# Optimization experiments

Measured on AMD Instinct MI355X. Metric: run time of the kernel, lower is better.

Reference implementation:

```python
import jax, jax.numpy as jnp
import numpy as np

BQ, BK = 128, 64  # SpargeAttn-style Q/K block sizes
NEG = -1e30


def _block_mask(q, k, simthreshd1, cdfthreshd, scale):
    """Mean-similarity block selection: a (q-block, k-block) pair is pruned only
    when both blocks are self-similar (mean cosine sim to block mean exceeds the
    per-head simthreshd1) AND it is not in the top-CDF mass (cdfthreshd) of the
    compressed block-level softmax."""
    B, H, L, D = q.shape
    nq, nk = L // BQ, L // BK
    qb = q.reshape(B, H, nq, BQ, D)
    kb = k.reshape(B, H, nk, BK, D)
    qm = qb.mean(3)  # [B,H,nq,D] block means
    km = kb.mean(3)  # [B,H,nk,D]

    def blocksim(xb, xm):
        xn = xb / (jnp.linalg.norm(xb, axis=-1, keepdims=True) + 1e-6)
        mn = xm / (jnp.linalg.norm(xm, axis=-1, keepdims=True) + 1e-6)
        return jnp.einsum('bhntd,bhnd->bhnt', xn, mn).mean(-1)  # [B,H,n]

    th = simthreshd1[None, :, None]
    comp_q = blocksim(qb, qm) > th  # [B,H,nq] self-similar q blocks
    comp_k = blocksim(kb, km) > th  # [B,H,nk]

    # compressed attention over block means, then CDF-based top-mass selection
    p = jax.nn.softmax(jnp.einsum('bhqd,bhkd->bhqk', qm, km) * scale, axis=-1)
    order = jnp.argsort(-p, axis=-1)
    sp = jnp.take_along_axis(p, order, axis=-1)
    csum = jnp.cumsum(sp, axis=-1)
    keep_sorted = (csum - sp) < cdfthreshd[None, :, None, None]  # prefix covering tau
    rank = jnp.argsort(order, axis=-1)  # inverse permutation
    selected = jnp.take_along_axis(keep_sorted, rank, axis=-1)  # [B,H,nq,nk]

    return selected | ~(comp_q[..., :, None] & comp_k[..., None, :])


def setup_inputs() -> dict:
    key = jax.random.key(0)
    kq, kk, kv, kc = jax.random.split(key, 4)
    B, H, L, D = 1, 16, 2048, 64
    return {
        'q': jax.random.normal(kq, (B, H, L, D), dtype=jnp.float32),
        'k': jax.random.normal(kk, (B, H, L, D), dtype=jnp.float32),
        'v': jax.random.normal(kv, (B, H, L, D), dtype=jnp.float32),
        'simthreshd1': jnp.zeros((H,), dtype=jnp.float32),
        'cdfthreshd': jax.random.uniform(kc, (H,), dtype=jnp.float32),
    }


def reference(q, k, v, simthreshd1, cdfthreshd):
    B, H, L, D = q.shape
    scale = 1.0 / np.sqrt(D).astype(np.float32)
    # smooth_k: subtract per-(B,H) key mean (softmax-invariant shift, matches kernel)
    k = k - k.mean(axis=-2, keepdims=True)
    bmask = _block_mask(q, k, simthreshd1, cdfthreshd, scale)  # [B,H,nq,nk] bool
    mask_tok = jnp.repeat(jnp.repeat(bmask, BQ, axis=2), BK, axis=3)  # [B,H,L,L]
    s = jnp.einsum('bhqd,bhkd->bhqk', q, k) * scale
    s = jnp.where(mask_tok, s, NEG)
    p = jax.nn.softmax(s, axis=-1)
    return jnp.einsum('bhqk,bhkd->bhqd', p, v)
```

## Files before the change

kernel.cpp:

```cpp
#include <hip/hip_runtime.h>

#define HH 16
#define LL 2048
#define DD 64
#define BQ 128
#define BK 64
#define NQ (LL/BQ)
#define NK (LL/BK)
#define SCALE 0.125f
#define QSCALE (0.125f * 1.44269504f)

typedef __attribute__((ext_vector_type(8))) short s8v;
typedef __attribute__((ext_vector_type(4))) float f4v;

static __device__ __forceinline__ ushort f2bf(float x) {
    unsigned u = __float_as_uint(x);
    u += 0x7fff + ((u >> 16) & 1);
    return (ushort)(u >> 16);
}

__global__ void kmean1_kernel(const float* __restrict__ k, float* __restrict__ kpart) {
    int b = blockIdx.x;
    int h = blockIdx.y;
    int t = threadIdx.x;
    int d = t & 63, c = t >> 6;
    const float* kh = k + ((size_t)h*LL + (size_t)b*256) * DD;
    float s = 0.f;
    for (int l = c*64; l < c*64 + 64; ++l) s += kh[(size_t)l * DD + d];
    __shared__ float red[4][64];
    red[c][d] = s;
    __syncthreads();
    if (t < 64) kpart[((size_t)h*8 + b)*64 + t] = red[0][t]+red[1][t]+red[2][t]+red[3][t];
}

__global__ __launch_bounds__(128) void stats_kernel(
        const float* __restrict__ q, const float* __restrict__ k, const float* __restrict__ v,
        const float* __restrict__ kpart, const float* __restrict__ simth,
        float* __restrict__ qm, float* __restrict__ km,
        int* __restrict__ compq, int* __restrict__ compk,
        ushort* __restrict__ qb, ushort* __restrict__ kb, ushort* __restrict__ vTb) {
    __shared__ __align__(16) char smem[34304];
    int h = blockIdx.y, t = threadIdx.x;

    if ((int)blockIdx.x < NQ) {
        int qi = blockIdx.x;
        float (*xs)[DD+1] = (float(*)[DD+1])smem;
        float* mean = (float*)(smem + 33280);
        float* red  = (float*)(smem + 33536);
        size_t row = (size_t)h*LL + (size_t)qi*BQ + t;
        const float* rp = q + row * DD;
        float x[DD]; float n2 = 0.f;
        #pragma unroll
        for (int d = 0; d < DD; d += 4) {
            float4 v4 = *(const float4*)(rp + d);
            x[d]=v4.x; x[d+1]=v4.y; x[d+2]=v4.z; x[d+3]=v4.w;
            n2 += v4.x*v4.x + v4.y*v4.y + v4.z*v4.z + v4.w*v4.w;
        }
        #pragma unroll
        for (int d = 0; d < DD; d += 4) {
            ushort4 o;
            o.x = f2bf(x[d]*QSCALE);   o.y = f2bf(x[d+1]*QSCALE);
            o.z = f2bf(x[d+2]*QSCALE); o.w = f2bf(x[d+3]*QSCALE);
            *(ushort4*)(qb + row*DD + d) = o;
        }
        #pragma unroll
        for (int d = 0; d < DD; ++d) xs[t][d] = x[d];
        __syncthreads();
        {
            int d = t & 63, hf = t >> 6;
            float s = 0.f;
            for (int r = hf*64; r < hf*64 + 64; ++r) s += xs[r][d];
            red[t] = s;
        }
        __syncthreads();
        if (t < DD) mean[t] = (red[t] + red[64 + t]) * (1.0f/BQ);
        __syncthreads();
        float dot = 0.f, m2 = 0.f;
        #pragma unroll
        for (int d = 0; d < DD; ++d) { dot += x[d]*mean[d]; m2 += mean[d]*mean[d]; }
        float cs = dot / ((sqrtf(n2) + 1e-6f) * (sqrtf(m2) + 1e-6f));
        __syncthreads();
        red[t] = cs; __syncthreads();
        for (int sft = BQ/2; sft > 0; sft >>= 1) {
            if (t < sft) red[t] += red[t + sft];
            __syncthreads();
        }
        if (t == 0) compq[h*NQ + qi] = (red[0] * (1.0f/BQ)) > simth[h] ? 1 : 0;
        if (t < DD) qm[((size_t)h*NQ + qi)*DD + t] = mean[t];
    } else {
        int ki = blockIdx.x - NQ;
        float* mu_s = (float*)smem;
        float (*xs)[DD+1] = (float(*)[DD+1])(smem + 256);
        ushort (*vs)[66]  = (ushort(*)[66])(smem + 256 + 16640);
        float* mean = (float*)(smem + 256 + 16640 + 8448);
        float* red  = (float*)(smem + 256 + 16640 + 8448 + 256);
        if (t < 64) {
            float s = 0.f;
            #pragma unroll
            for (int b = 0; b < 8; ++b) s += kpart[((size_t)h*8 + b)*64 + t];
            mu_s[t] = s * (1.0f/LL);
        }
        __syncthreads();
        size_t rowb = (size_t)h*LL + (size_t)ki*BK;
        float x[DD]; float n2 = 0.f;
        if (t < 64) {
            const float* rp = k + (rowb + t) * DD;
            #pragma unroll
            for (int d = 0; d < DD; d += 4) {
                float4 v4 = *(const float4*)(rp + d);
                v4.x -= mu_s[d]; v4.y -= mu_s[d+1]; v4.z -= mu_s[d+2]; v4.w -= mu_s[d+3];
                x[d]=v4.x; x[d+1]=v4.y; x[d+2]=v4.z; x[d+3]=v4.w;
                n2 += v4.x*v4.x + v4.y*v4.y + v4.z*v4.z + v4.w*v4.w;
            }
            #pragma unroll
            for (int d = 0; d < DD; d += 4) {
                ushort4 o;
                o.x = f2bf(x[d]);   o.y = f2bf(x[d+1]);
                o.z = f2bf(x[d+2]); o.w = f2bf(x[d+3]);
                *(ushort4*)(kb + (rowb + t)*DD + d) = o;
            }
            #pragma unroll
            for (int d = 0; d < DD; ++d) xs[t][d] = x[d];
        } else {
            int tk = t - 64;
            const float* vp = v + (rowb + tk) * DD;
            #pragma unroll
            for (int d = 0; d < DD; d += 4) {
                float4 v4 = *(const float4*)(vp + d);
                vs[tk][d]   = f2bf(v4.x); vs[tk][d+1] = f2bf(v4.y);
                vs[tk][d+2] = f2bf(v4.z); vs[tk][d+3] = f2bf(v4.w);
            }
        }
        __syncthreads();
        if (t < 64) {
            size_t vbase = ((size_t)h*DD + t)*LL + (size_t)ki*64;
            #pragma unroll
            for (int r8 = 0; r8 < 64; r8 += 8) {
                s8v o;
                #pragma unroll
                for (int e = 0; e < 8; ++e) o[e] = (short)vs[r8+e][t];
                *(s8v*)(vTb + vbase + r8) = o;
            }
            float s = 0.f;
            for (int r = 0; r < BK; ++r) s += xs[r][t];
            mean[t] = s * (1.0f/BK);
        }
        __syncthreads();
        if (t < 64) {
            float dot = 0.f, m2 = 0.f;
            #pragma unroll
            for (int d = 0; d < DD; ++d) { dot += x[d]*mean[d]; m2 += mean[d]*mean[d]; }
            float cs = dot / ((sqrtf(n2) + 1e-6f) * (sqrtf(m2) + 1e-6f));
            red[t] = cs;
        }
        __syncthreads();
        for (int sft = 32; sft > 0; sft >>= 1) {
            if (t < sft) red[t] += red[t + sft];
            __syncthreads();
        }
        if (t == 0) compk[h*NK + ki] = (red[0] * (1.0f/BK)) > simth[h] ? 1 : 0;
        if (t < 64) km[((size_t)h*NK + ki)*DD + t] = mean[t];
    }
}

__global__ void bmask_kernel(const float* __restrict__ qm, const float* __restrict__ km,
                             const int* __restrict__ compq, const int* __restrict__ compk,
                             const float* __restrict__ cdfth, unsigned* __restrict__ bmaskbits) {
    int qi = blockIdx.x, h = blockIdx.y;
    int j = threadIdx.x;
    __shared__ float ssh[NK];
    __shared__ float p[NK];
    const float* qv = qm + ((size_t)h*NQ + qi)*DD;
    const float* kv = km + ((size_t)h*NK + j)*DD;
    float s = 0.f;
    for (int d = 0; d < DD; ++d) s += qv[d]*kv[d];
    ssh[j] = s * SCALE;
    __syncthreads();
    float m = ssh[0];
    for (int i = 1; i < NK; ++i) m = fmaxf(m, ssh[i]);
    float den = 0.f;
    for (int i = 0; i < NK; ++i) den += expf(ssh[i] - m);
    p[j] = expf(ssh[j] - m) / den;
    __syncthreads();
    float pj = p[j];
    float mass = 0.f;
    for (int i = 0; i < NK; ++i) {
        float pi = p[i];
        if (pi > pj || (pi == pj && i < j)) mass += pi;
    }
    int sel = (mass < cdfth[h]) ? 1 : 0;
    int keep = (sel || !(compq[h*NQ+qi] && compk[h*NK+j])) ? 1 : 0;
    unsigned long long bal = __ballot(keep);
    if (j == 0) bmaskbits[h*NQ + qi] = (unsigned)bal;
}

__global__ __launch_bounds__(256, 2) void attn_kernel(
        const ushort* __restrict__ qb, const ushort* __restrict__ kb,
        const ushort* __restrict__ vTb, const unsigned* __restrict__ bmaskbits,
        float* __restrict__ out) {
    __shared__ __align__(16) char shmem[69632];
    ushort* pl = (ushort*)shmem + (threadIdx.x >> 6) * 64 * 72;
    float*  Ob = (float*)shmem;
    float*  mb = (float*)(shmem + 67584);
    float*  lb = (float*)(shmem + 68608);

    int bid  = blockIdx.x;
    int slot = bid >> 3;
    int h    = ((slot >> 5) << 3) | (bid & 7);
    int qi   = (slot & 31) >> 1;
    int half = slot & 1;
    int tid  = threadIdx.x;
    int w    = tid >> 6;
    int l    = tid & 63;
    int lo = l & 15, hi = l >> 4;
    int r0 = qi*BQ + half*64;

    unsigned msk = bmaskbits[h*NQ + qi];

    const ushort* qh = qb  + (size_t)h*LL*DD;
    const ushort* kh = kb  + (size_t)h*LL*DD;
    const ushort* vh = vTb + (size_t)h*DD*LL;

    s8v qf[4][2];
    #pragma unroll
    for (int qt = 0; qt < 4; ++qt)
        #pragma unroll
        for (int kk = 0; kk < 2; ++kk)
            qf[qt][kk] = *(const s8v*)(qh + (size_t)(r0 + qt*16 + lo)*DD + kk*32 + hi*8);

    f4v O[4][4];
    float m[4], lsum[4];
    #pragma unroll
    for (int qt = 0; qt < 4; ++qt) {
        m[qt] = -1e30f; lsum[qt] = 0.f;
        #pragma unroll
        for (int dt = 0; dt < 4; ++dt) O[qt][dt] = (f4v){0.f,0.f,0.f,0.f};
    }

    unsigned mm = msk; int rank = 0;
    while (mm) {
        int j = __ffs(mm) - 1; mm &= mm - 1;
        if (((rank++) & 3) != w) continue;

        const ushort* kbj = kh + (size_t)j*BK*DD;
        const ushort* vbj = vh + (size_t)j*BK;

        s8v kf[4][2];
        #pragma unroll
        for (int kt = 0; kt < 4; ++kt)
            #pragma unroll
            for (int kk = 0; kk < 2; ++kk)
                kf[kt][kk] = *(const s8v*)(kbj + (size_t)(kt*16 + lo)*DD + kk*32 + hi*8);

        f4v S[4][4];
        #pragma unroll
        for (int kt = 0; kt < 4; ++kt)
            #pragma unroll
            for (int qt = 0; qt < 4; ++qt)
                S[kt][qt] = (f4v){0.f,0.f,0.f,0.f};
        __builtin_amdgcn_s_setprio(1);
        #pragma unroll
        for (int kk = 0; kk < 2; ++kk)
            #pragma unroll
            for (int kt = 0; kt < 4; ++kt)
                #pragma unroll
                for (int qt = 0; qt < 4; ++qt)
                    S[kt][qt] = __builtin_amdgcn_mfma_f32_16x16x32_bf16(kf[kt][kk], qf[qt][kk], S[kt][qt], 0, 0, 0);
        __builtin_amdgcn_s_setprio(0);

        s8v vf[2][4];
        #pragma unroll
        for (int kk = 0; kk < 2; ++kk)
            #pragma unroll
            for (int dt = 0; dt < 4; ++dt)
                vf[kk][dt] = *(const s8v*)(vbj + (size_t)(dt*16 + lo)*LL + kk*32 + hi*8);

        float pm[4];
        #pragma unroll
        for (int qt = 0; qt < 4; ++qt) {
            float a0 = fmaxf(fmaxf(S[0][qt][0],S[0][qt][1]), fmaxf(S[0][qt][2],S[0][qt][3]));
            float a1 = fmaxf(fmaxf(S[1][qt][0],S[1][qt][1]), fmaxf(S[1][qt][2],S[1][qt][3]));
            float a2 = fmaxf(fmaxf(S[2][qt][0],S[2][qt][1]), fmaxf(S[2][qt][2],S[2][qt][3]));
            float a3 = fmaxf(fmaxf(S[3][qt][0],S[3][qt][1]), fmaxf(S[3][qt][2],S[3][qt][3]));
            float p = fmaxf(fmaxf(a0,a1), fmaxf(a2,a3));
            p = fmaxf(p, __shfl_xor(p, 16));
            p = fmaxf(p, __shfl_xor(p, 32));
            pm[qt] = p;
        }
        bool grow = (pm[0] > m[0]+8.0f) | (pm[1] > m[1]+8.0f) |
                    (pm[2] > m[2]+8.0f) | (pm[3] > m[3]+8.0f);
        if (__any(grow)) {
            float alpha[4];
            #pragma unroll
            for (int qt = 0; qt < 4; ++qt) {
                float mn = fmaxf(m[qt], pm[qt]);
                alpha[qt] = __builtin_amdgcn_exp2f(m[qt] - mn);
                lsum[qt] *= alpha[qt];
                m[qt] = mn;
            }
            #pragma unroll
            for (int qt = 0; qt < 4; ++qt)
                #pragma unroll
                for (int r = 0; r < 4; ++r) {
                    float a = __shfl(alpha[qt], hi*4 + r);
                    #pragma unroll
                    for (int dt = 0; dt < 4; ++dt) O[qt][dt][r] *= a;
                }
        }
        #pragma unroll
        for (int qt = 0; qt < 4; ++qt) {
            float ps = 0.f;
            #pragma unroll
            for (int kt = 0; kt < 4; ++kt) {
                float p0 = __builtin_amdgcn_exp2f(S[kt][qt][0] - m[qt]);
                float p1 = __builtin_amdgcn_exp2f(S[kt][qt][1] - m[qt]);
                float p2 = __builtin_amdgcn_exp2f(S[kt][qt][2] - m[qt]);
                float p3 = __builtin_amdgcn_exp2f(S[kt][qt][3] - m[qt]);
                ps += (p0 + p1) + (p2 + p3);
                unsigned c01, c23;
                asm("v_cvt_pk_bf16_f32 %0, %1, %2" : "=v"(c01) : "v"(p0), "v"(p1));
                asm("v_cvt_pk_bf16_f32 %0, %1, %2" : "=v"(c23) : "v"(p2), "v"(p3));
                *(uint2*)&pl[(qt*16 + lo)*72 + kt*16 + hi*4] = make_uint2(c01, c23);
            }
            lsum[qt] += ps;
        }
        __builtin_amdgcn_s_setprio(1);
        #pragma unroll
        for (int qt = 0; qt < 4; ++qt)
            #pragma unroll
            for (int kk = 0; kk < 2; ++kk) {
                s8v pa = *(const s8v*)&pl[(qt*16 + lo)*72 + kk*32 + hi*8];
                #pragma unroll
                for (int dt = 0; dt < 4; ++dt)
                    O[qt][dt] = __builtin_amdgcn_mfma_f32_16x16x32_bf16(pa, vf[kk][dt], O[qt][dt], 0, 0, 0);
            }
        __builtin_amdgcn_s_setprio(0);
    }

    #pragma unroll
    for (int qt = 0; qt < 4; ++qt) {
        lsum[qt] += __shfl_xor(lsum[qt], 16);
        lsum[qt] += __shfl_xor(lsum[qt], 32);
    }

    __syncthreads();

    if (hi == 0) {
        #pragma unroll
        for (int qt = 0; qt < 4; ++qt) {
            mb[w*64 + qt*16 + lo] = m[qt];
            lb[w*64 + qt*16 + lo] = lsum[qt];
        }
    }
    #pragma unroll
    for (int qt = 0; qt < 4; ++qt)
        #pragma unroll
        for (int dt = 0; dt < 4; ++dt)
            #pragma unroll
            for (int r = 0; r < 4; ++r)
                Ob[w*4224 + (qt*16 + hi*4 + r)*66 + dt*16 + lo] = O[qt][dt][r];
    __syncthreads();

    {
        int q = l;
        float mw0 = mb[q], mw1 = mb[64+q], mw2 = mb[128+q], mw3 = mb[192+q];
        float ms = fmaxf(fmaxf(mw0,mw1), fmaxf(mw2,mw3));
        float c0 = __builtin_amdgcn_exp2f(mw0 - ms);
        float c1 = __builtin_amdgcn_exp2f(mw1 - ms);
        float c2 = __builtin_amdgcn_exp2f(mw2 - ms);
        float c3 = __builtin_amdgcn_exp2f(mw3 - ms);
        float ls = lb[q]*c0 + lb[64+q]*c1 + lb[128+q]*c2 + lb[192+q]*c3;
        float inv = 1.0f / ls;
        float* orow = out + ((size_t)h*LL + r0 + q)*DD + w*16;
        #pragma unroll
        for (int i4 = 0; i4 < 4; ++i4) {
            float4 o;
            #pragma unroll
            for (int e = 0; e < 4; ++e) {
                int d = w*16 + i4*4 + e;
                float acc = Ob[q*66 + d]*c0 + Ob[4224 + q*66 + d]*c1
                          + Ob[8448 + q*66 + d]*c2 + Ob[12672 + q*66 + d]*c3;
                ((float*)&o)[e] = acc * inv;
            }
            *(float4*)(orow + i4*4) = o;
        }
    }
}

extern "C" void kernel_launch(void* const* d_in, const int* in_sizes, int n_in,
                              void* d_out, int out_size, void* d_ws, size_t ws_size,
                              hipStream_t stream) {
    const float* q     = (const float*)d_in[0];
    const float* k     = (const float*)d_in[1];
    const float* v     = (const float*)d_in[2];
    const float* simth = (const float*)d_in[3];
    const float* cdfth = (const float*)d_in[4];
    float* out = (float*)d_out;

    float* ws    = (float*)d_ws;
    float* kpart = ws;
    float* qm    = kpart + HH*8*64;
    float* km    = qm + HH*NQ*DD;
    int*   compq = (int*)(km + HH*NK*DD);
    int*   compk = compq + HH*NQ;
    unsigned* bmb = (unsigned*)(compk + HH*NK);
    size_t off = (size_t)((char*)(bmb + HH*NQ) - (char*)d_ws);
    off = (off + 15) & ~(size_t)15;
    ushort* qbuf = (ushort*)((char*)d_ws + off);
    ushort* kbuf = qbuf + (size_t)HH*LL*DD;
    ushort* vTb  = kbuf + (size_t)HH*LL*DD;

    kmean1_kernel<<<dim3(8, HH), 256, 0, stream>>>(k, kpart);
    stats_kernel<<<dim3(NQ + NK, HH), 128, 0, stream>>>(q, k, v, kpart, simth,
                                                        qm, km, compq, compk,
                                                        qbuf, kbuf, vTb);
    bmask_kernel<<<dim3(NQ, HH), NK, 0, stream>>>(qm, km, compq, compk, cdfth, bmb);
    attn_kernel<<<dim3(NQ*2*HH), 256, 0, stream>>>(qbuf, kbuf, vTb, bmb, out);
}
```

Before: 75.43 us.

## Fuse block-mask computation into stats kernel via cooperative grid sync

Removes the separate bmask kernel launch and runs the block-selection logic at the end of the stats kernel, after a cooperative-groups grid-wide barrier. The aim is to save one kernel launch and its launch gap. In exchange it adds a grid sync plus thread fences and needs a cooperative launch, which requires all 768 blocks to be co-resident. The grid sync itself may cost as much as the launch it replaces.

```diff
diff --git a/kernel.cpp b/kernel.cpp
--- a/kernel.cpp
+++ b/kernel.cpp
@@ -1,4 +1,7 @@
 #include <hip/hip_runtime.h>
+#include <hip/hip_cooperative_groups.h>
+
+namespace cg = cooperative_groups;
 
 #define HH 16
 #define LL 2048
@@ -33,12 +36,13 @@
     if (t < 64) kpart[((size_t)h*8 + b)*64 + t] = red[0][t]+red[1][t]+red[2][t]+red[3][t];
 }
 
-__global__ __launch_bounds__(128) void stats_kernel(
+__global__ __launch_bounds__(128, 2) void stats_kernel(
         const float* __restrict__ q, const float* __restrict__ k, const float* __restrict__ v,
         const float* __restrict__ kpart, const float* __restrict__ simth,
         float* __restrict__ qm, float* __restrict__ km,
         int* __restrict__ compq, int* __restrict__ compk,
-        ushort* __restrict__ qb, ushort* __restrict__ kb, ushort* __restrict__ vTb) {
+        ushort* __restrict__ qb, ushort* __restrict__ kb, ushort* __restrict__ vTb,
+        const float* __restrict__ cdfth, unsigned* __restrict__ bmaskbits) {
     __shared__ __align__(16) char smem[34304];
     int h = blockIdx.y, t = threadIdx.x;
 
@@ -161,37 +165,45 @@
         if (t == 0) compk[h*NK + ki] = (red[0] * (1.0f/BK)) > simth[h] ? 1 : 0;
         if (t < 64) km[((size_t)h*NK + ki)*DD + t] = mean[t];
     }
-}
-
-__global__ void bmask_kernel(const float* __restrict__ qm, const float* __restrict__ km,
-                             const int* __restrict__ compq, const int* __restrict__ compk,
-                             const float* __restrict__ cdfth, unsigned* __restrict__ bmaskbits) {
-    int qi = blockIdx.x, h = blockIdx.y;
-    int j = threadIdx.x;
-    __shared__ float ssh[NK];
-    __shared__ float p[NK];
-    const float* qv = qm + ((size_t)h*NQ + qi)*DD;
-    const float* kv = km + ((size_t)h*NK + j)*DD;
-    float s = 0.f;
-    for (int d = 0; d < DD; ++d) s += qv[d]*kv[d];
-    ssh[j] = s * SCALE;
-    __syncthreads();
-    float m = ssh[0];
-    for (int i = 1; i < NK; ++i) m = fmaxf(m, ssh[i]);
-    float den = 0.f;
-    for (int i = 0; i < NK; ++i) den += expf(ssh[i] - m);
-    p[j] = expf(ssh[j] - m) / den;
-    __syncthreads();
-    float pj = p[j];
-    float mass = 0.f;
-    for (int i = 0; i < NK; ++i) {
-        float pi = p[i];
-        if (pi > pj || (pi == pj && i < j)) mass += pi;
-    }
-    int sel = (mass < cdfth[h]) ? 1 : 0;
-    int keep = (sel || !(compq[h*NQ+qi] && compk[h*NK+j])) ? 1 : 0;
-    unsigned long long bal = __ballot(keep);
-    if (j == 0) bmaskbits[h*NQ + qi] = (unsigned)bal;
+
+    __threadfence();
+    cg::this_grid().sync();
+    __threadfence();
+
+    int b = blockIdx.y * gridDim.x + blockIdx.x;
+    if (b < NQ*HH) {
+        int h2 = b >> 4, qi2 = b & 15;
+        float* ssh = (float*)smem;
+        float* pp  = ssh + 32;
+        if (t < NK) {
+            const float* qv = qm + ((size_t)h2*NQ + qi2)*DD;
+            const float* kv = km + ((size_t)h2*NK + t)*DD;
+            float s = 0.f;
+            for (int d = 0; d < DD; ++d) s += qv[d]*kv[d];
+            ssh[t] = s * SCALE;
+        }
+        __syncthreads();
+        if (t < NK) {
+            float m = ssh[0];
+            for (int i = 1; i < NK; ++i) m = fmaxf(m, ssh[i]);
+            float den = 0.f;
+            for (int i = 0; i < NK; ++i) den += expf(ssh[i] - m);
+            pp[t] = expf(ssh[t] - m) / den;
+        }
+        __syncthreads();
+        if (t < NK) {
+            float pj = pp[t];
+            float mass = 0.f;
+            for (int i = 0; i < NK; ++i) {
+                float pi = pp[i];
+                if (pi > pj || (pi == pj && i < t)) mass += pi;
+            }
+            int sel = (mass < cdfth[h2]) ? 1 : 0;
+            int keep = (sel || !(compq[h2*NQ+qi2] && compk[h2*NK+t])) ? 1 : 0;
+            unsigned long long bal = __ballot(keep);
+            if (t == 0) bmaskbits[h2*NQ + qi2] = (unsigned)bal;
+        }
+    }
 }
 
 __global__ __launch_bounds__(256, 2) void attn_kernel(
@@ -411,9 +423,18 @@
     ushort* vTb  = kbuf + (size_t)HH*LL*DD;
 
     kmean1_kernel<<<dim3(8, HH), 256, 0, stream>>>(k, kpart);
-    stats_kernel<<<dim3(NQ + NK, HH), 128, 0, stream>>>(q, k, v, kpart, simth,
-                                                        qm, km, compq, compk,
-                                                        qbuf, kbuf, vTb);
-    bmask_kernel<<<dim3(NQ, HH), NK, 0, stream>>>(qm, km, compq, compk, cdfth, bmb);
+
+    {
+        void* args[] = {
+            (void*)&q, (void*)&k, (void*)&v, (void*)&kpart, (void*)&simth,
+            (void*)&qm, (void*)&km, (void*)&compq, (void*)&compk,
+            (void*)&qbuf, (void*)&kbuf, (void*)&vTb,
+            (void*)&cdfth, (void*)&bmb
+        };
+        hipLaunchCooperativeKernel((const void*)stats_kernel,
+                                   dim3(NQ + NK, HH), dim3(128),
+                                   args, 0, stream);
+    }
+
     attn_kernel<<<dim3(NQ*2*HH), 256, 0, stream>>>(qbuf, kbuf, vTb, bmb, out);
 }
```

Result: slower. 264.3 us (+250.3%).

## Fuse block-mask computation into stats kernel via last-block atomic counter

Applied to the files above, without the earlier changes.

Removes the separate bmask kernel launch. Each stats block bumps a per-head atomic counter, and the last block to finish for a head computes that head's block mask over all q-blocks. The mask is built by four 32-thread groups, and each 64-bit ballot is split to pick that group's 32 bits. The counter is reset in the first kernel. This trades one launch gap and dependency bubble for a serialized tail, where one block per head loops over 16 q-blocks.

```diff
diff --git a/kernel.cpp b/kernel.cpp
--- a/kernel.cpp
+++ b/kernel.cpp
@@ -19,10 +19,12 @@
     return (ushort)(u >> 16);
 }
 
-__global__ void kmean1_kernel(const float* __restrict__ k, float* __restrict__ kpart) {
+__global__ void kmean1_kernel(const float* __restrict__ k, float* __restrict__ kpart,
+                              int* __restrict__ cnt) {
     int b = blockIdx.x;
     int h = blockIdx.y;
     int t = threadIdx.x;
+    if (b == 0 && t == 0) cnt[h] = 0;
     int d = t & 63, c = t >> 6;
     const float* kh = k + ((size_t)h*LL + (size_t)b*256) * DD;
     float s = 0.f;
@@ -38,7 +40,9 @@
         const float* __restrict__ kpart, const float* __restrict__ simth,
         float* __restrict__ qm, float* __restrict__ km,
         int* __restrict__ compq, int* __restrict__ compk,
-        ushort* __restrict__ qb, ushort* __restrict__ kb, ushort* __restrict__ vTb) {
+        ushort* __restrict__ qb, ushort* __restrict__ kb, ushort* __restrict__ vTb,
+        const float* __restrict__ cdfth, unsigned* __restrict__ bmaskbits,
+        int* __restrict__ cnt) {
     __shared__ __align__(16) char smem[34304];
     int h = blockIdx.y, t = threadIdx.x;
 
@@ -161,37 +165,51 @@
         if (t == 0) compk[h*NK + ki] = (red[0] * (1.0f/BK)) > simth[h] ? 1 : 0;
         if (t < 64) km[((size_t)h*NK + ki)*DD + t] = mean[t];
     }
-}
-
-__global__ void bmask_kernel(const float* __restrict__ qm, const float* __restrict__ km,
-                             const int* __restrict__ compq, const int* __restrict__ compk,
-                             const float* __restrict__ cdfth, unsigned* __restrict__ bmaskbits) {
-    int qi = blockIdx.x, h = blockIdx.y;
-    int j = threadIdx.x;
-    __shared__ float ssh[NK];
-    __shared__ float p[NK];
-    const float* qv = qm + ((size_t)h*NQ + qi)*DD;
-    const float* kv = km + ((size_t)h*NK + j)*DD;
-    float s = 0.f;
-    for (int d = 0; d < DD; ++d) s += qv[d]*kv[d];
-    ssh[j] = s * SCALE;
+
+    __shared__ int lastFlag;
+    __threadfence();
     __syncthreads();
-    float m = ssh[0];
-    for (int i = 1; i < NK; ++i) m = fmaxf(m, ssh[i]);
-    float den = 0.f;
-    for (int i = 0; i < NK; ++i) den += expf(ssh[i] - m);
-    p[j] = expf(ssh[j] - m) / den;
+    if (t == 0) {
+        int old = atomicAdd(&cnt[h], 1);
+        lastFlag = (old == NQ + NK - 1) ? 1 : 0;
+    }
     __syncthreads();
-    float pj = p[j];
-    float mass = 0.f;
-    for (int i = 0; i < NK; ++i) {
-        float pi = p[i];
-        if (pi > pj || (pi == pj && i < j)) mass += pi;
-    }
-    int sel = (mass < cdfth[h]) ? 1 : 0;
-    int keep = (sel || !(compq[h*NQ+qi] && compk[h*NK+j])) ? 1 : 0;
-    unsigned long long bal = __ballot(keep);
-    if (j == 0) bmaskbits[h*NQ + qi] = (unsigned)bal;
+    if (lastFlag) {
+        __threadfence();
+        int grp = t >> 5, j = t & 31;
+        float* ssh = (float*)smem + grp*64;
+        float* pp  = ssh + 32;
+        for (int qq = grp; qq < NQ; qq += 4) {
+            const float* qv = qm + ((size_t)h*NQ + qq)*DD;
+            const float* kv = km + ((size_t)h*NK + j)*DD;
+            float s = 0.f;
+            for (int d = 0; d < DD; ++d) s += qv[d]*kv[d];
+            ssh[j] = s * SCALE;
+            __syncthreads();
+            {
+                float m = ssh[0];
+                for (int i = 1; i < NK; ++i) m = fmaxf(m, ssh[i]);
+                float den = 0.f;
+                for (int i = 0; i < NK; ++i) den += expf(ssh[i] - m);
+                pp[j] = expf(ssh[j] - m) / den;
+            }
+            __syncthreads();
+            {
+                float pj = pp[j];
+                float mass = 0.f;
+                for (int i = 0; i < NK; ++i) {
+                    float pi = pp[i];
+                    if (pi > pj || (pi == pj && i < j)) mass += pi;
+                }
+                int sel = (mass < cdfth[h]) ? 1 : 0;
+                int keep = (sel || !(compq[h*NQ+qq] && compk[h*NK+j])) ? 1 : 0;
+                unsigned long long bal = __ballot(keep);
+                unsigned msk32 = (grp & 1) ? (unsigned)(bal >> 32) : (unsigned)bal;
+                if (j == 0) bmaskbits[h*NQ + qq] = msk32;
+            }
+            __syncthreads();
+        }
+    }
 }
 
 __global__ __launch_bounds__(256, 2) void attn_kernel(
@@ -404,16 +422,17 @@
     int*   compq = (int*)(km + HH*NK*DD);
     int*   compk = compq + HH*NQ;
     unsigned* bmb = (unsigned*)(compk + HH*NK);
-    size_t off = (size_t)((char*)(bmb + HH*NQ) - (char*)d_ws);
+    int*   cnt   = (int*)(bmb + HH*NQ);
+    size_t off = (size_t)((char*)(cnt + HH) - (char*)d_ws);
     off = (off + 15) & ~(size_t)15;
     ushort* qbuf = (ushort*)((char*)d_ws + off);
     ushort* kbuf = qbuf + (size_t)HH*LL*DD;
     ushort* vTb  = kbuf + (size_t)HH*LL*DD;
 
-    kmean1_kernel<<<dim3(8, HH), 256, 0, stream>>>(k, kpart);
+    kmean1_kernel<<<dim3(8, HH), 256, 0, stream>>>(k, kpart, cnt);
     stats_kernel<<<dim3(NQ + NK, HH), 128, 0, stream>>>(q, k, v, kpart, simth,
                                                         qm, km, compq, compk,
-                                                        qbuf, kbuf, vTb);
-    bmask_kernel<<<dim3(NQ, HH), NK, 0, stream>>>(qm, km, compq, compk, cdfth, bmb);
+                                                        qbuf, kbuf, vTb,
+                                                        cdfth, bmb, cnt);
     attn_kernel<<<dim3(NQ*2*HH), 256, 0, stream>>>(qbuf, kbuf, vTb, bmb, out);
 }
```

After: 150.5 us. +99.5%, slower.
